# Optimization experiments

Measured on AMD Instinct MI355X. Metric: run time of the kernel, lower is better.

Reference implementation:

```python
import jax, jax.numpy as jnp
import numpy as np

WS = 16      # window_size
OWS = 24     # overlap_win_size = int(16*0.5) + 16
PAD = 4      # (OWS - WS) // 2
NH = 6       # num_heads
DIM = 192
MLP_HID = 384  # dim * mlp_ratio(2)
TABLE = (WS + OWS - 1) ** 2  # 1521


def _ln(x, g, b, eps=1e-5):
    m = x.mean(-1, keepdims=True)
    v = ((x - m) ** 2).mean(-1, keepdims=True)
    return (x - m) * jax.lax.rsqrt(v + eps) * g + b


def setup_inputs() -> dict:
    key = jax.random.key(0)
    ks = jax.random.split(key, 16)
    B, H, W, C = 1, 192, 192, DIM
    x = jax.random.normal(ks[0], (B, H * W, C), jnp.float32)
    rpi = jax.random.randint(ks[1], (WS * WS, OWS * OWS), 0, TABLE, dtype=jnp.int64)
    s = 0.02
    return {
        "x": x,
        "rpi": rpi,
        "h": H,
        "w": W,
        "norm1_g": jnp.ones((C,), jnp.float32),
        "norm1_b": jnp.zeros((C,), jnp.float32),
        "qkv_w": jax.random.normal(ks[2], (C, 3 * C), jnp.float32) * s,
        "qkv_b": jnp.zeros((3 * C,), jnp.float32),
        "rpb_table": jax.random.normal(ks[3], (TABLE, NH), jnp.float32) * s,
        "proj_w": jax.random.normal(ks[4], (C, C), jnp.float32) * s,
        "proj_b": jnp.zeros((C,), jnp.float32),
        "norm2_g": jnp.ones((C,), jnp.float32),
        "norm2_b": jnp.zeros((C,), jnp.float32),
        "fc1_w": jax.random.normal(ks[5], (C, MLP_HID), jnp.float32) * s,
        "fc1_b": jnp.zeros((MLP_HID,), jnp.float32),
        "fc2_w": jax.random.normal(ks[6], (MLP_HID, C), jnp.float32) * s,
        "fc2_b": jnp.zeros((C,), jnp.float32),
    }


def reference(x, rpi, h, w, norm1_g, norm1_b, qkv_w, qkv_b, rpb_table,
              proj_w, proj_b, norm2_g, norm2_b, fc1_w, fc1_b, fc2_w, fc2_b):
    B, L, C = x.shape
    d = C // NH
    scale = d ** -0.5
    nhw, nww = h // WS, w // WS
    nW = nhw * nww

    shortcut = x
    xn = _ln(x, norm1_g, norm1_b).reshape(B, h, w, C)
    qkv = xn @ qkv_w + qkv_b                       # (B, h, w, 3C)
    q, k, v = jnp.split(qkv, 3, axis=-1)

    # non-overlapping query windows: (B*nW, WS*WS, C)
    qw = q.reshape(B, nhw, WS, nww, WS, C).transpose(0, 1, 3, 2, 4, 5)
    qw = qw.reshape(B * nW, WS * WS, C)

    # overlapping key/value windows via padded gather (equiv. to nn.Unfold)
    ri = (jnp.arange(nhw) * WS)[:, None] + jnp.arange(OWS)[None, :]  # (nhw, OWS)
    ci = (jnp.arange(nww) * WS)[:, None] + jnp.arange(OWS)[None, :]  # (nww, OWS)

    def win(t):
        tp = jnp.pad(t, ((0, 0), (PAD, PAD), (PAD, PAD), (0, 0)))
        g = tp[:, ri[:, :, None, None], ci[None, None, :, :], :]     # (B,nhw,OWS,nww,OWS,C)
        return g.transpose(0, 1, 3, 2, 4, 5).reshape(B * nW, OWS * OWS, C)

    kw, vw = win(k), win(v)

    qh = qw.reshape(B * nW, WS * WS, NH, d).transpose(0, 2, 1, 3) * scale
    kh = kw.reshape(B * nW, OWS * OWS, NH, d).transpose(0, 2, 1, 3)
    vh = vw.reshape(B * nW, OWS * OWS, NH, d).transpose(0, 2, 1, 3)

    attn = jnp.einsum('bhqd,bhkd->bhqk', qh, kh)
    bias = rpb_table[rpi.reshape(-1)].reshape(WS * WS, OWS * OWS, NH)
    bias = bias.transpose(2, 0, 1)                 # (NH, nq, n)
    attn = jax.nn.softmax(attn + bias[None], axis=-1)
    out = jnp.einsum('bhqk,bhkd->bhqd', attn, vh)
    out = out.transpose(0, 2, 1, 3).reshape(B * nW, WS * WS, C)

    # window reverse
    xr = out.reshape(B, nhw, nww, WS, WS, C).transpose(0, 1, 3, 2, 4, 5)
    xr = xr.reshape(B, h * w, C)

    x2 = xr @ proj_w + proj_b + shortcut
    x3 = _ln(x2, norm2_g, norm2_b)
    mlp = jax.nn.gelu(x3 @ fc1_w + fc1_b, approximate=False) @ fc2_w + fc2_b
    return x2 + mlp
```

## Files before the change

### kernel.cpp

```cpp
#include <hip/hip_runtime.h>
#include <hip/hip_bf16.h>

#define NH 6
#define DIM 192
#define HW 192
#define M_TOK (HW*HW)
#define QSC 0.25503488f
#define L2E 1.4426950408889634f

typedef __attribute__((ext_vector_type(8))) __bf16 bf16x8;
typedef __attribute__((ext_vector_type(8))) short short8;
typedef __attribute__((ext_vector_type(4))) short s16x4;
typedef __attribute__((ext_vector_type(4))) float floatx4;

__device__ inline unsigned short f2bf(float f) {
    union { float f; unsigned int u; } v; v.f = f;
    unsigned int r = (v.u + 0x7FFFu + ((v.u >> 16) & 1u)) >> 16;
    return (unsigned short)r;
}
__device__ inline short f2bfh(float f) {
    __bf16 b = (__bf16)f;
    return __builtin_bit_cast(short, b);
}
__device__ inline float exp2fast(float x) {
#if __has_builtin(__builtin_amdgcn_exp2f)
    return __builtin_amdgcn_exp2f(x);
#else
    return exp2f(x);
#endif
}
__device__ inline floatx4 bf4f(s16x4 b) {
    floatx4 f;
    #pragma unroll
    for (int r = 0; r < 4; r++) {
        union { unsigned u; float f; } v;
        v.u = ((unsigned)(unsigned short)b[r]) << 16;
        f[r] = v.f;
    }
    return f;
}

__device__ inline floatx4 mfma16(short8 a, short8 b, floatx4 c) {
    return __builtin_amdgcn_mfma_f32_16x16x32_bf16(
        __builtin_bit_cast(bf16x8, a), __builtin_bit_cast(bf16x8, b), c, 0, 0, 0);
}

template <int OFF>
__device__ inline s16x4 tr16(unsigned addr) {
    s16x4 r;
    asm volatile("ds_read_b64_tr_b16 %0, %1 offset:%2"
                 : "=&v"(r) : "v"(addr), "i"(OFF));
    return r;
}
template <int OFF>
__device__ inline s16x4 tr16m(unsigned addr) {
    s16x4 r;
    asm volatile("ds_read_b64_tr_b16 %0, %1 offset:%2"
                 : "=&v"(r) : "v"(addr), "i"(OFF) : "memory");
    return r;
}
template <int N>
__device__ __forceinline__ void wait_lgkm() {
    asm volatile("s_waitcnt lgkmcnt(%0)" :: "i"(N) : "memory");
}
__device__ inline short8 cat8(s16x4 a, s16x4 b) {
    return __builtin_shufflevector(a, b, 0, 1, 2, 3, 4, 5, 6, 7);
}

__device__ __forceinline__ void gload16(const void* g, unsigned lds_off) {
    __builtin_amdgcn_global_load_lds(
        (const __attribute__((address_space(1))) unsigned int*)(uintptr_t)g,
        (__attribute__((address_space(3))) unsigned int*)(uintptr_t)lds_off,
        16, 0, 0);
}

__device__ __forceinline__ void btfrag_body(int id, const int* __restrict__ rpi,
                                            const float* __restrict__ table,
                                            unsigned short* __restrict__ btf) {
    int lane = id & 63;
    int t = id >> 6;
    int kt = t % 36; t /= 36;
    int qt = t & 15; int hh = t >> 4;
    int k = kt * 16 + (lane & 15);
    int qb = qt * 16 + (lane >> 4) * 4;
    s16x4 v;
    #pragma unroll
    for (int r = 0; r < 4; r++)
        v[r] = f2bfh(table[rpi[(qb + r) * 576 + k] * NH + hh] * L2E);
    *(s16x4*)&btf[(size_t)id * 4] = v;
}

__device__ __forceinline__ void wcast_rest_body(int i2, const float* __restrict__ projw,
                                                const float* __restrict__ fc1w,
                                                const float* __restrict__ fc2w,
                                                unsigned short* __restrict__ wt_proj,
                                                unsigned short* __restrict__ wt_fc1,
                                                unsigned short* __restrict__ wt_fc2) {
    if (i2 < 36864) {
        int n = i2 / 192, k = i2 - n * 192;
        wt_proj[i2] = f2bf(projw[k * 192 + n]);
    } else if (i2 < 110592) {
        int i = i2 - 36864;
        int n = i / 192, k = i - n * 192;
        wt_fc1[i] = f2bf(fc1w[k * 384 + n]);
    } else {
        int i = i2 - 110592;
        int n = i / 384, k = i - n * 384;
        wt_fc2[i] = f2bf(fc2w[k * 192 + n]);
    }
}

__global__ __launch_bounds__(256) void prep_kernel(
    const float* __restrict__ qkvw,
    const float* __restrict__ x, const float* __restrict__ n1g,
    const float* __restrict__ n1b,
    unsigned short* __restrict__ wt_qkv,
    unsigned short* __restrict__ xn) {
    int bid = blockIdx.x;
    if (bid < 432) {
        int id = bid * 256 + threadIdx.x;
        int n = id / 192, k = id - n * 192;
        wt_qkv[id] = f2bf(qkvw[k * 576 + n]);
    } else {
        int row = (bid - 432) * 4 + (threadIdx.x >> 6);
        int lane = threadIdx.x & 63;
        const float* r = x + (size_t)row * DIM;
        float x0 = r[lane], x1 = r[lane + 64], x2 = r[lane + 128];
        float s = x0 + x1 + x2;
        #pragma unroll
        for (int m = 32; m >= 1; m >>= 1) s += __shfl_xor(s, m);
        float mean = s * (1.f / 192.f);
        float d0 = x0 - mean, d1 = x1 - mean, d2 = x2 - mean;
        float v = d0 * d0 + d1 * d1 + d2 * d2;
        #pragma unroll
        for (int m = 32; m >= 1; m >>= 1) v += __shfl_xor(v, m);
        float rstd = rsqrtf(v * (1.f / 192.f) + 1e-5f);
        unsigned short* o = xn + (size_t)row * DIM;
        o[lane]       = f2bf(d0 * rstd * n1g[lane]       + n1b[lane]);
        o[lane + 64]  = f2bf(d1 * rstd * n1g[lane + 64]  + n1b[lane + 64]);
        o[lane + 128] = f2bf(d2 * rstd * n1g[lane + 128] + n1b[lane + 128]);
    }
}

template <int MODE, int KK>
__global__ __launch_bounds__(256, 4) void gemm_kernel(
    const unsigned short* __restrict__ A,
    const unsigned short* __restrict__ Wt,
    const float* __restrict__ bias,
    void* __restrict__ outp,
    int N,
    const int* __restrict__ rpi, const float* __restrict__ table,
    unsigned short* __restrict__ btf,
    const float* __restrict__ projw, const float* __restrict__ fc1w,
    const float* __restrict__ fc2w,
    unsigned short* __restrict__ wt_proj, unsigned short* __restrict__ wt_fc1,
    unsigned short* __restrict__ wt_fc2) {
    if (MODE == 0 && blockIdx.y >= 9) {
        int extra = (blockIdx.y - 9) * 288 + blockIdx.x;
        if (extra < 864) {
            btfrag_body(extra * 256 + threadIdx.x, rpi, table, btf);
        } else if (extra < 1584) {
            wcast_rest_body((extra - 864) * 256 + threadIdx.x,
                            projw, fc1w, fc2w, wt_proj, wt_fc1, wt_fc2);
        }
        return;
    }
    __shared__ __align__(16) short sAB[19968];
    constexpr int STAGES = KK / 96;
    int tid = threadIdx.x;
    int w = tid >> 6, lane = tid & 63;
    int bm = blockIdx.x, bn = blockIdx.y;
    int lr = lane & 15, h = lane >> 4;
    floatx4 acc[2][4];
    #pragma unroll
    for (int i = 0; i < 2; i++)
        #pragma unroll
        for (int j = 0; j < 4; j++) acc[i][j] = (floatx4){0.f, 0.f, 0.f, 0.f};

    unsigned ldsbase = (unsigned)(uintptr_t)&sAB[0];

    for (int s = 0; s < STAGES; s++) {
        if (s) __syncthreads();
        for (int W = w; W < 39; W += 4) {
            int o = W * 1024 + lane * 16;
            const unsigned short* src;
            if (o < 26624) {
                int r = o / 208;
                int c = (o - r * 208) >> 4; c = c < 12 ? c : 11;
                src = &A[(size_t)(bm * 128 + r) * KK + s * 96 + c * 8];
            } else {
                int o2 = o - 26624;
                int r = o2 / 208;
                int c = (o2 - r * 208) >> 4; c = c < 12 ? c : 11;
                src = &Wt[(size_t)(bn * 64 + r) * KK + s * 96 + c * 8];
            }
            gload16(src, ldsbase + (unsigned)(W * 1024));
        }
        __syncthreads();
        #pragma unroll
        for (int kk = 0; kk < 3; kk++) {
            int kc = (kk * 4 + h) * 8;
            short8 a0 = *(const short8*)&sAB[(w * 32 + lr) * 104 + kc];
            short8 a1 = *(const short8*)&sAB[(w * 32 + 16 + lr) * 104 + kc];
            short8 b0 = *(const short8*)&sAB[13312 + (lr) * 104 + kc];
            short8 b1 = *(const short8*)&sAB[13312 + (16 + lr) * 104 + kc];
            short8 b2 = *(const short8*)&sAB[13312 + (32 + lr) * 104 + kc];
            short8 b3 = *(const short8*)&sAB[13312 + (48 + lr) * 104 + kc];
            acc[0][0] = mfma16(a0, b0, acc[0][0]);
            acc[0][1] = mfma16(a0, b1, acc[0][1]);
            acc[0][2] = mfma16(a0, b2, acc[0][2]);
            acc[0][3] = mfma16(a0, b3, acc[0][3]);
            acc[1][0] = mfma16(a1, b0, acc[1][0]);
            acc[1][1] = mfma16(a1, b1, acc[1][1]);
            acc[1][2] = mfma16(a1, b2, acc[1][2]);
            acc[1][3] = mfma16(a1, b3, acc[1][3]);
        }
    }

    int rowbase = bm * 128 + w * 32 + h * 4;
    int colbase = bn * 64;
    #pragma unroll
    for (int mi = 0; mi < 2; mi++) {
        #pragma unroll
        for (int ni = 0; ni < 4; ni++) {
            int c = colbase + ni * 16 + lr;
            float bv = bias[c];
            #pragma unroll
            for (int j = 0; j < 4; j++) {
                int r = rowbase + mi * 16 + j;
                float v = acc[mi][ni][j] + bv;
                if (MODE == 0) {
                    int part = c / 192;
                    int rem = c - part * 192;
                    int hd = rem >> 5, d = rem & 31;
                    if (part == 0) v *= QSC;
                    ((unsigned short*)outp)[((size_t)(part * 6 + hd) * M_TOK + r) * 32 + d] = f2bf(v);
                } else if (MODE == 2) {
                    size_t idx = (size_t)r * N + c;
                    float gl = 0.5f * v * (1.f + erff(v * 0.70710678118654752f));
                    ((unsigned short*)outp)[idx] = f2bf(gl);
                } else {
                    size_t idx = (size_t)r * N + c;
                    ((float*)outp)[idx] = v + ((float*)outp)[idx];
                }
            }
        }
    }
}

__global__ __launch_bounds__(256, 3) void projln_kernel(
    const unsigned short* __restrict__ A,
    const unsigned short* __restrict__ Wt,
    const float* __restrict__ bias,
    const float* __restrict__ res,
    const float* __restrict__ g2, const float* __restrict__ b2,
    float* __restrict__ x2out,
    unsigned short* __restrict__ xnout) {
    __shared__ __align__(16) short sAB[26624];
    int tid = threadIdx.x;
    int w = tid >> 6, lane = tid & 63;
    int bm = blockIdx.x;
    int lr = lane & 15, h = lane >> 4;
    floatx4 acc[12];
    #pragma unroll
    for (int ni = 0; ni < 12; ni++) acc[ni] = (floatx4){0.f, 0.f, 0.f, 0.f};

    unsigned ldsbase = (unsigned)(uintptr_t)&sAB[0];

    for (int s = 0; s < 2; s++) {
        if (s) __syncthreads();
        for (int W = w; W < 52; W += 4) {
            int o = W * 1024 + lane * 16;
            const unsigned short* src;
            if (o < 13312) {
                int r = o / 208;
                int c = (o - r * 208) >> 4; c = c < 12 ? c : 11;
                int col = s * 96 + c * 8;
                int hd = col >> 5, d = col & 31;
                src = &A[((size_t)hd * M_TOK + bm * 64 + r) * 32 + d];
            } else {
                int o2 = o - 13312;
                int r = o2 / 208;
                int c = (o2 - r * 208) >> 4; c = c < 12 ? c : 11;
                src = &Wt[(size_t)r * 192 + s * 96 + c * 8];
            }
            gload16(src, ldsbase + (unsigned)(W * 1024));
        }
        __syncthreads();
        #pragma unroll
        for (int kk = 0; kk < 3; kk++) {
            int kc = (kk * 4 + h) * 8;
            short8 a0 = *(const short8*)&sAB[(w * 16 + lr) * 104 + kc];
            #pragma unroll
            for (int ni = 0; ni < 12; ni++) {
                short8 bfr = *(const short8*)&sAB[6656 + (ni * 16 + lr) * 104 + kc];
                acc[ni] = mfma16(a0, bfr, acc[ni]);
            }
        }
    }

    int row0 = bm * 64 + w * 16 + h * 4;
    float s1[4] = {0.f, 0.f, 0.f, 0.f}, s2[4] = {0.f, 0.f, 0.f, 0.f};
    #pragma unroll
    for (int ni = 0; ni < 12; ni++) {
        int c = ni * 16 + lr;
        float bv = bias[c];
        #pragma unroll
        for (int j = 0; j < 4; j++) {
            size_t idx = (size_t)(row0 + j) * 192 + c;
            float v = acc[ni][j] + bv + res[idx];
            acc[ni][j] = v;
            s1[j] += v;
            s2[j] += v * v;
        }
    }
    #pragma unroll
    for (int mask = 1; mask <= 8; mask <<= 1) {
        #pragma unroll
        for (int j = 0; j < 4; j++) {
            s1[j] += __shfl_xor(s1[j], mask);
            s2[j] += __shfl_xor(s2[j], mask);
        }
    }
    float mean[4], rstd[4];
    #pragma unroll
    for (int j = 0; j < 4; j++) {
        mean[j] = s1[j] * (1.f / 192.f);
        float var = s2[j] * (1.f / 192.f) - mean[j] * mean[j];
        rstd[j] = rsqrtf(var + 1e-5f);
    }
    #pragma unroll
    for (int ni = 0; ni < 12; ni++) {
        int c = ni * 16 + lr;
        float gw = g2[c], bw = b2[c];
        #pragma unroll
        for (int j = 0; j < 4; j++) {
            size_t idx = (size_t)(row0 + j) * 192 + c;
            float v = acc[ni][j];
            x2out[idx] = v;
            xnout[idx] = f2bf((v - mean[j]) * rstd[j] * gw + bw);
        }
    }
}

__global__ __launch_bounds__(256, 3) void attn_mfma_kernel(
    const unsigned short* __restrict__ qkv,
    const unsigned short* __restrict__ btf,
    unsigned short* __restrict__ out) {
    __shared__ __align__(16) short sK[2][2304];
    __shared__ __align__(16) short sV[2][2048];
    __shared__ __align__(16) short sPt[4][4096];
    int win = blockIdx.x, head = blockIdx.y;
    int iy = win / 12, ix = win % 12;
    int tid = threadIdx.x;
    int w = tid >> 6, lane = tid & 63;
    int m = lane & 15, h = lane >> 4;

    const unsigned short* Qp = qkv + (size_t)head * M_TOK * 32;
    const unsigned short* Kp = qkv + (size_t)(6 + head) * M_TOK * 32;

    short8 qf[4];
    #pragma unroll
    for (int i = 0; i < 4; i++) {
        int wy = w * 4 + i;
        size_t tok = (size_t)(iy * 16 + wy) * HW + ix * 16 + m;
        qf[i] = *(const short8*)&Qp[tok * 32 + h * 8];
    }

    short ob = (m == 0) ? (short)0x3F80 : (short)0;
    short8 bones = {ob, ob, ob, ob, ob, ob, ob, ob};

    floatx4 oacc[4][2];
    floatx4 lacc[4];
    #pragma unroll
    for (int i = 0; i < 4; i++) {
        lacc[i] = (floatx4){0.f, 0.f, 0.f, 0.f};
        oacc[i][0] = (floatx4){0.f, 0.f, 0.f, 0.f};
        oacc[i][1] = (floatx4){0.f, 0.f, 0.f, 0.f};
    }

    int skey = tid >> 2, dq = tid & 3;
    short* kdst = &sK[0][skey * 36 + dq * 8];
    short* vdst = &sV[0][(dq >> 1) * 1024 + (skey >> 2) * 64 + (skey & 3) * 16 + (dq & 1) * 8];

    auto fetch = [&](int c, short8& kv, short8& vv) {
        int key = c * 64 + skey;
        int oy = key / 24, ox = key - (key / 24) * 24;
        int gy = iy * 16 - 4 + oy, gx = ix * 16 - 4 + ox;
        kv = (short8){0,0,0,0,0,0,0,0};
        vv = (short8){0,0,0,0,0,0,0,0};
        if (gy >= 0 && gy < HW && gx >= 0 && gx < HW) {
            const unsigned short* p = &Kp[((size_t)gy * HW + gx) * 32 + dq * 8];
            kv = *(const short8*)p;
            vv = *(const short8*)(p + 6 * M_TOK * 32);
        }
    };

    {
        short8 kv, vv;
        fetch(0, kv, vv);
        *(short8*)kdst = kv;
        *(short8*)vdst = vv;
    }

    unsigned sPbase = (unsigned)(uintptr_t)&sPt[w][0];
    unsigned sPa = sPbase + 8 * m + 256 * h;
    unsigned sVa0 = (unsigned)(uintptr_t)&sV[0][0] + 8 * m + 256 * h;
    char* sPwb = (char*)&sPt[w][0] + 128 * (m >> 2) + 32 * (m & 3) + 8 * h;

    for (int c = 0; c < 9; c++) {
        __syncthreads();
        int cur = c & 1;
        short8 knx, vnx;
        bool more = (c < 8);
        if (more) fetch(c + 1, knx, vnx);

        const short* sKc = sK[cur];
        short8 kfrag[4];
        #pragma unroll
        for (int kt = 0; kt < 4; kt++)
            kfrag[kt] = *(const short8*)&sKc[(kt * 16 + m) * 36 + h * 8];

        const unsigned short* bb = btf + ((((size_t)head * 16 + w * 4) * 36 + c * 4) * 64 + lane) * 4;

        #pragma unroll
        for (int i = 0; i < 4; i++) {
            floatx4 s[4];
            #pragma unroll
            for (int kt = 0; kt < 4; kt++)
                s[kt] = bf4f(*(const s16x4*)&bb[(size_t)(i * 36 + kt) * 256]);
            #pragma unroll
            for (int kt = 0; kt < 4; kt++)
                s[kt] = mfma16(qf[i], kfrag[kt], s[kt]);
            #pragma unroll
            for (int kt = 0; kt < 4; kt++) {
                s16x4 pk;
                #pragma unroll
                for (int r = 0; r < 4; r++)
                    pk[r] = f2bfh(exp2fast(s[kt][r]));
                *(s16x4*)(sPwb + i * 2048 + kt * 512) = pk;
            }
        }

        unsigned sVa = sVa0 + cur * 4096;
        short8 vb[4];
        {
            s16x4 lo0 = tr16<0>(sVa),    hi0 = tr16<128>(sVa);
            s16x4 lo1 = tr16<2048>(sVa), hi1 = tr16<2176>(sVa);
            s16x4 lo2 = tr16<1024>(sVa), hi2 = tr16<1152>(sVa);
            s16x4 lo3 = tr16<3072>(sVa), hi3 = tr16<3200>(sVa);
            vb[0] = cat8(lo0, hi0);
            vb[1] = cat8(lo1, hi1);
            vb[2] = cat8(lo2, hi2);
            vb[3] = cat8(lo3, hi3);
        }
        s16x4 pl0 = tr16m<0>(sPa),    ph0 = tr16m<128>(sPa);
        s16x4 pl1 = tr16m<1024>(sPa), ph1 = tr16m<1152>(sPa);
        #pragma unroll
        for (int i = 0; i < 4; i++) {
            s16x4 nl0, nh0, nl1, nh1;
            if (i < 3) {
                unsigned a = sPa + (unsigned)((i + 1) * 2048);
                nl0 = tr16m<0>(a);    nh0 = tr16m<128>(a);
                nl1 = tr16m<1024>(a); nh1 = tr16m<1152>(a);
                wait_lgkm<4>();
            } else {
                wait_lgkm<0>();
            }
            __builtin_amdgcn_sched_barrier(0);
            short8 pa0 = cat8(pl0, ph0);
            short8 pa1 = cat8(pl1, ph1);
            oacc[i][0] = mfma16(pa0, vb[0], oacc[i][0]);
            oacc[i][1] = mfma16(pa0, vb[1], oacc[i][1]);
            oacc[i][0] = mfma16(pa1, vb[2], oacc[i][0]);
            oacc[i][1] = mfma16(pa1, vb[3], oacc[i][1]);
            lacc[i] = mfma16(pa0, bones, lacc[i]);
            lacc[i] = mfma16(pa1, bones, lacc[i]);
            if (i < 3) { pl0 = nl0; ph0 = nh0; pl1 = nl1; ph1 = nh1; }
        }

        if (more) {
            int nb = 1 - cur;
            *(short8*)(kdst + nb * 2304) = knx;
            *(short8*)(vdst + nb * 2048) = vnx;
        }
    }

    unsigned short* Op = out + (size_t)head * M_TOK * 32;
    #pragma unroll
    for (int i = 0; i < 4; i++) {
        float inv[4];
        #pragma unroll
        for (int r = 0; r < 4; r++) {
            float sum = __shfl(lacc[i][r], lane & 48);
            inv[r] = 1.f / sum;
        }
        int wy = w * 4 + i;
        #pragma unroll
        for (int dt = 0; dt < 2; dt++)
            #pragma unroll
            for (int r = 0; r < 4; r++) {
                size_t tok = (size_t)(iy * 16 + wy) * HW + ix * 16 + h * 4 + r;
                Op[tok * 32 + dt * 16 + m] = f2bf(oacc[i][dt][r] * inv[r]);
            }
    }
}

extern "C" void kernel_launch(void* const* d_in, const int* in_sizes, int n_in,
                              void* d_out, int out_size, void* d_ws, size_t ws_size,
                              hipStream_t stream) {
    const float* x     = (const float*)d_in[0];
    const int*   rpi   = (const int*)d_in[1];
    const float* n1g   = (const float*)d_in[4];
    const float* n1b   = (const float*)d_in[5];
    const float* qkvw  = (const float*)d_in[6];
    const float* qkvb  = (const float*)d_in[7];
    const float* rpb   = (const float*)d_in[8];
    const float* projw = (const float*)d_in[9];
    const float* projb = (const float*)d_in[10];
    const float* n2g   = (const float*)d_in[11];
    const float* n2b   = (const float*)d_in[12];
    const float* fc1w  = (const float*)d_in[13];
    const float* fc1b  = (const float*)d_in[14];
    const float* fc2w  = (const float*)d_in[15];
    const float* fc2b  = (const float*)d_in[16];

    char* ws = (char*)d_ws;
    unsigned short* wt_qkv  = (unsigned short*)ws;
    unsigned short* wt_proj = wt_qkv + 110592;
    unsigned short* wt_fc1  = wt_proj + 36864;
    unsigned short* wt_fc2  = wt_fc1 + 73728;
    unsigned short* btf     = (unsigned short*)(ws + 589824);
    unsigned short* xn      = (unsigned short*)(ws + 4128768);
    unsigned short* qkv     = (unsigned short*)(ws + 18284544);
    unsigned short* attn_o  = (unsigned short*)(ws + 60751872);

    prep_kernel<<<9648, 256, 0, stream>>>(qkvw, x, n1g, n1b, wt_qkv, xn);
    gemm_kernel<0, 192><<<dim3(288, 15), 256, 0, stream>>>(
        xn, wt_qkv, qkvb, qkv, 576,
        rpi, rpb, btf, projw, fc1w, fc2w, wt_proj, wt_fc1, wt_fc2);
    attn_mfma_kernel<<<dim3(144, 6), 256, 0, stream>>>(qkv, btf, attn_o);
    projln_kernel<<<576, 256, 0, stream>>>(
        attn_o, wt_proj, projb, x, n2g, n2b, (float*)d_out, xn);
    gemm_kernel<2, 192><<<dim3(288, 6), 256, 0, stream>>>(
        xn, wt_fc1, fc1b, qkv, 384,
        nullptr, nullptr, nullptr, nullptr, nullptr, nullptr, nullptr, nullptr, nullptr);
    gemm_kernel<3, 384><<<dim3(288, 3), 256, 0, stream>>>(
        qkv, wt_fc2, fc2b, d_out, 192,
        nullptr, nullptr, nullptr, nullptr, nullptr, nullptr, nullptr, nullptr, nullptr);
}
```

Before: 151.1 us.

## Fuse proj+LN2, fc1+GELU and fc2 into one per-tile mega kernel

Replaces the projection+LayerNorm kernel and the two MLP GEMM launches with a single kernel. Each 64-row tile computes proj plus residual and LN2 into LDS, then runs fc1+GELU in 96-column chunks and accumulates fc2 into registers before writing the output once. This removes the global round-trips for x2, the normalized activations and the 384-wide hidden tensor, plus two launches. In exchange, weights are restaged many times per block with frequent barriers, there is no load/compute overlap, and only 576 blocks run at lower occupancy.

```diff
diff --git a/kernel.cpp b/kernel.cpp
--- a/kernel.cpp
+++ b/kernel.cpp
@@ -235,110 +235,171 @@
                     int hd = rem >> 5, d = rem & 31;
                     if (part == 0) v *= QSC;
                     ((unsigned short*)outp)[((size_t)(part * 6 + hd) * M_TOK + r) * 32 + d] = f2bf(v);
-                } else if (MODE == 2) {
-                    size_t idx = (size_t)r * N + c;
-                    float gl = 0.5f * v * (1.f + erff(v * 0.70710678118654752f));
-                    ((unsigned short*)outp)[idx] = f2bf(gl);
-                } else {
-                    size_t idx = (size_t)r * N + c;
-                    ((float*)outp)[idx] = v + ((float*)outp)[idx];
                 }
             }
         }
     }
 }
 
-__global__ __launch_bounds__(256, 3) void projln_kernel(
-    const unsigned short* __restrict__ A,
-    const unsigned short* __restrict__ Wt,
-    const float* __restrict__ bias,
+__global__ __launch_bounds__(256, 2) void mega_kernel(
+    const unsigned short* __restrict__ Aop,
+    const unsigned short* __restrict__ Wp,
+    const unsigned short* __restrict__ W1,
+    const unsigned short* __restrict__ W2,
+    const float* __restrict__ pb,
+    const float* __restrict__ b1,
+    const float* __restrict__ b2f,
     const float* __restrict__ res,
-    const float* __restrict__ g2, const float* __restrict__ b2,
-    float* __restrict__ x2out,
-    unsigned short* __restrict__ xnout) {
-    __shared__ __align__(16) short sAB[26624];
+    const float* __restrict__ g2, const float* __restrict__ bb2,
+    float* __restrict__ outp) {
+    __shared__ __align__(16) short sA[13312];
+    __shared__ __align__(16) short sH[6656];
+    __shared__ __align__(16) short sB[10240];
     int tid = threadIdx.x;
     int w = tid >> 6, lane = tid & 63;
     int bm = blockIdx.x;
     int lr = lane & 15, h = lane >> 4;
-    floatx4 acc[12];
-    #pragma unroll
-    for (int ni = 0; ni < 12; ni++) acc[ni] = (floatx4){0.f, 0.f, 0.f, 0.f};
-
-    unsigned ldsbase = (unsigned)(uintptr_t)&sAB[0];
-
-    for (int s = 0; s < 2; s++) {
-        if (s) __syncthreads();
-        for (int W = w; W < 52; W += 4) {
+    int lrow0 = w * 16 + h * 4;
+    int row0 = bm * 64 + lrow0;
+
+    floatx4 x2a[12];
+    #pragma unroll
+    for (int t = 0; t < 12; t++) x2a[t] = (floatx4){0.f, 0.f, 0.f, 0.f};
+
+    auto stageB = [&](const unsigned short* base, int stride) {
+        unsigned ldsB = (unsigned)(uintptr_t)&sB[0];
+        #pragma unroll
+        for (int W = 0; W < 5; W++) {
+            int Wc = W * 4 + w;
+            int o = Wc * 1024 + lane * 16;
+            int r = o / 208;
+            int c = (o - r * 208) >> 4; c = c < 12 ? c : 11;
+            if (r > 95) { r = 95; c = 11; }
+            gload16(&base[r * stride + c * 8], ldsB + (unsigned)(Wc * 1024));
+        }
+    };
+
+    {
+        unsigned ldsA = (unsigned)(uintptr_t)&sA[0];
+        for (int W = w; W < 26; W += 4) {
             int o = W * 1024 + lane * 16;
-            const unsigned short* src;
-            if (o < 13312) {
-                int r = o / 208;
-                int c = (o - r * 208) >> 4; c = c < 12 ? c : 11;
-                int col = s * 96 + c * 8;
-                int hd = col >> 5, d = col & 31;
-                src = &A[((size_t)hd * M_TOK + bm * 64 + r) * 32 + d];
-            } else {
-                int o2 = o - 13312;
-                int r = o2 / 208;
-                int c = (o2 - r * 208) >> 4; c = c < 12 ? c : 11;
-                src = &Wt[(size_t)r * 192 + s * 96 + c * 8];
-            }
-            gload16(src, ldsbase + (unsigned)(W * 1024));
-        }
-        __syncthreads();
-        #pragma unroll
-        for (int kk = 0; kk < 3; kk++) {
-            int kc = (kk * 4 + h) * 8;
-            short8 a0 = *(const short8*)&sAB[(w * 16 + lr) * 104 + kc];
-            #pragma unroll
-            for (int ni = 0; ni < 12; ni++) {
-                short8 bfr = *(const short8*)&sAB[6656 + (ni * 16 + lr) * 104 + kc];
-                acc[ni] = mfma16(a0, bfr, acc[ni]);
-            }
-        }
-    }
-
-    int row0 = bm * 64 + w * 16 + h * 4;
-    float s1[4] = {0.f, 0.f, 0.f, 0.f}, s2[4] = {0.f, 0.f, 0.f, 0.f};
-    #pragma unroll
-    for (int ni = 0; ni < 12; ni++) {
-        int c = ni * 16 + lr;
-        float bv = bias[c];
+            int sl = o / 13312;
+            int o2 = o - sl * 13312;
+            int r = o2 / 208;
+            int c = (o2 - r * 208) >> 4; c = c < 12 ? c : 11;
+            int col = sl * 96 + c * 8;
+            int hd = col >> 5, d = col & 31;
+            gload16(&Aop[((size_t)hd * M_TOK + bm * 64 + r) * 32 + d],
+                    ldsA + (unsigned)(W * 1024));
+        }
+    }
+
+#define GEMM6(ACCBASE, SAPTR) { \
+    _Pragma("unroll") for (int kk = 0; kk < 3; kk++) { int kc = (kk * 4 + h) * 8; \
+        short8 a_ = *(const short8*)&(SAPTR)[(w * 16 + lr) * 104 + kc]; \
+        _Pragma("unroll") for (int ni = 0; ni < 6; ni++) { \
+            short8 b_ = *(const short8*)&sB[(ni * 16 + lr) * 104 + kc]; \
+            x2a[(ACCBASE) + ni] = mfma16(a_, b_, x2a[(ACCBASE) + ni]); } } }
+
+#define GEMMH(SAPTR) { \
+    _Pragma("unroll") for (int kk = 0; kk < 3; kk++) { int kc = (kk * 4 + h) * 8; \
+        short8 a_ = *(const short8*)&(SAPTR)[(w * 16 + lr) * 104 + kc]; \
+        _Pragma("unroll") for (int ni = 0; ni < 6; ni++) { \
+            short8 b_ = *(const short8*)&sB[(ni * 16 + lr) * 104 + kc]; \
+            ha[ni] = mfma16(a_, b_, ha[ni]); } } }
+
+    stageB(Wp, 192);
+    __syncthreads();
+    GEMM6(0, sA);
+    __syncthreads(); stageB(Wp + 96, 192); __syncthreads();
+    GEMM6(0, sA + 6656);
+    __syncthreads(); stageB(Wp + 96 * 192, 192); __syncthreads();
+    GEMM6(6, sA);
+    __syncthreads(); stageB(Wp + 96 * 192 + 96, 192); __syncthreads();
+    GEMM6(6, sA + 6656);
+
+    {
+        float s1[4] = {0.f, 0.f, 0.f, 0.f}, s2[4] = {0.f, 0.f, 0.f, 0.f};
+        #pragma unroll
+        for (int t = 0; t < 12; t++) {
+            int c = t * 16 + lr;
+            float bv = pb[c];
+            #pragma unroll
+            for (int j = 0; j < 4; j++) {
+                size_t idx = (size_t)(row0 + j) * 192 + c;
+                float v = x2a[t][j] + bv + res[idx];
+                x2a[t][j] = v;
+                s1[j] += v;
+                s2[j] += v * v;
+            }
+        }
+        #pragma unroll
+        for (int mask = 1; mask <= 8; mask <<= 1) {
+            #pragma unroll
+            for (int j = 0; j < 4; j++) {
+                s1[j] += __shfl_xor(s1[j], mask);
+                s2[j] += __shfl_xor(s2[j], mask);
+            }
+        }
+        float mean[4], rstd[4];
+        #pragma unroll
+        for (int j = 0; j < 4; j++) {
+            mean[j] = s1[j] * (1.f / 192.f);
+            float var = s2[j] * (1.f / 192.f) - mean[j] * mean[j];
+            rstd[j] = rsqrtf(var + 1e-5f);
+        }
+        #pragma unroll
+        for (int t = 0; t < 12; t++) {
+            int c = t * 16 + lr;
+            float gw = g2[c], bw = bb2[c];
+            int slab = t / 6;
+            int cc = c - slab * 96;
+            #pragma unroll
+            for (int j = 0; j < 4; j++) {
+                float lnv = (x2a[t][j] - mean[j]) * rstd[j] * gw + bw;
+                sA[slab * 6656 + (lrow0 + j) * 104 + cc] = f2bfh(lnv);
+            }
+        }
+    }
+
+    for (int q = 0; q < 4; q++) {
+        floatx4 ha[6];
+        #pragma unroll
+        for (int ni = 0; ni < 6; ni++) ha[ni] = (floatx4){0.f, 0.f, 0.f, 0.f};
+
+        __syncthreads(); stageB(W1 + (size_t)(q * 96) * 192, 192); __syncthreads();
+        GEMMH(sA);
+        __syncthreads(); stageB(W1 + (size_t)(q * 96) * 192 + 96, 192); __syncthreads();
+        GEMMH(sA + 6656);
+
+        #pragma unroll
+        for (int ni = 0; ni < 6; ni++) {
+            int c384 = q * 96 + ni * 16 + lr;
+            float bv = b1[c384];
+            #pragma unroll
+            for (int j = 0; j < 4; j++) {
+                float v = ha[ni][j] + bv;
+                float gl = 0.5f * v * (1.f + erff(v * 0.70710678118654752f));
+                sH[(lrow0 + j) * 104 + ni * 16 + lr] = f2bfh(gl);
+            }
+        }
+
+        __syncthreads(); stageB(W2 + q * 96, 384); __syncthreads();
+        GEMM6(0, sH);
+        __syncthreads(); stageB(W2 + (size_t)96 * 384 + q * 96, 384); __syncthreads();
+        GEMM6(6, sH);
+    }
+#undef GEMM6
+#undef GEMMH
+
+    #pragma unroll
+    for (int t = 0; t < 12; t++) {
+        int c = t * 16 + lr;
+        float bv = b2f[c];
         #pragma unroll
         for (int j = 0; j < 4; j++) {
             size_t idx = (size_t)(row0 + j) * 192 + c;
-            float v = acc[ni][j] + bv + res[idx];
-            acc[ni][j] = v;
-            s1[j] += v;
-            s2[j] += v * v;
-        }
-    }
-    #pragma unroll
-    for (int mask = 1; mask <= 8; mask <<= 1) {
-        #pragma unroll
-        for (int j = 0; j < 4; j++) {
-            s1[j] += __shfl_xor(s1[j], mask);
-            s2[j] += __shfl_xor(s2[j], mask);
-        }
-    }
-    float mean[4], rstd[4];
-    #pragma unroll
-    for (int j = 0; j < 4; j++) {
-        mean[j] = s1[j] * (1.f / 192.f);
-        float var = s2[j] * (1.f / 192.f) - mean[j] * mean[j];
-        rstd[j] = rsqrtf(var + 1e-5f);
-    }
-    #pragma unroll
-    for (int ni = 0; ni < 12; ni++) {
-        int c = ni * 16 + lr;
-        float gw = g2[c], bw = b2[c];
-        #pragma unroll
-        for (int j = 0; j < 4; j++) {
-            size_t idx = (size_t)(row0 + j) * 192 + c;
-            float v = acc[ni][j];
-            x2out[idx] = v;
-            xnout[idx] = f2bf((v - mean[j]) * rstd[j] * gw + bw);
+            outp[idx] = x2a[t][j] + bv;
         }
     }
 }
@@ -540,12 +601,7 @@
         xn, wt_qkv, qkvb, qkv, 576,
         rpi, rpb, btf, projw, fc1w, fc2w, wt_proj, wt_fc1, wt_fc2);
     attn_mfma_kernel<<<dim3(144, 6), 256, 0, stream>>>(qkv, btf, attn_o);
-    projln_kernel<<<576, 256, 0, stream>>>(
-        attn_o, wt_proj, projb, x, n2g, n2b, (float*)d_out, xn);
-    gemm_kernel<2, 192><<<dim3(288, 6), 256, 0, stream>>>(
-        xn, wt_fc1, fc1b, qkv, 384,
-        nullptr, nullptr, nullptr, nullptr, nullptr, nullptr, nullptr, nullptr, nullptr);
-    gemm_kernel<3, 384><<<dim3(288, 3), 256, 0, stream>>>(
-        qkv, wt_fc2, fc2b, d_out, 192,
-        nullptr, nullptr, nullptr, nullptr, nullptr, nullptr, nullptr, nullptr, nullptr);
-}
+    mega_kernel<<<576, 256, 0, stream>>>(
+        attn_o, wt_proj, wt_fc1, wt_fc2, projb, fc1b, fc2b,
+        x, n2g, n2b, (float*)d_out);
+}
```

Measured after the change: 154.1 us. 2.0% more time.
